# Performance work log

Measured on AMD Instinct MI355X. Metric: run time of the kernel, lower is better.

The kernel has to match this reference:

```python
import jax, jax.numpy as jnp
import numpy as np

N_NODES = 50000
N_EDGES = 1_600_000
DIMS = [512, 2048, 1024, 512]  # input, hiddens..., output
NEG_SLOPE = 0.2
EPS = 1e-12


def setup_inputs() -> dict:
    key = jax.random.key(0)
    ks = jax.random.split(key, 12)
    inp = {
        "x": jax.random.normal(ks[0], (N_NODES, DIMS[0]), dtype=jnp.float32),
        "edge_row": jax.random.randint(ks[1], (N_EDGES,), 0, N_NODES, dtype=jnp.int32),
        "edge_col": jax.random.randint(ks[2], (N_EDGES,), 0, N_NODES, dtype=jnp.int32),
        "edge_val": jax.random.uniform(ks[3], (N_EDGES,), dtype=jnp.float32),
    }
    # GraphConvolution params per layer: W [d_in, d_out], b [d_out]
    for i in range(len(DIMS) - 1):
        d_in, d_out = DIMS[i], DIMS[i + 1]
        scale = 1.0 / np.sqrt(d_in)
        inp[f"W{i}"] = jax.random.uniform(ks[4 + 2 * i], (d_in, d_out), minval=-scale, maxval=scale, dtype=jnp.float32)
        inp[f"b{i}"] = jnp.zeros((d_out,), dtype=jnp.float32)
    return inp


def _spmm(edge_row, edge_col, edge_val, h):
    # out[i] = sum_{e: row[e]==i} val[e] * h[col[e]]   (sparse adj @ h)
    msgs = edge_val[:, None] * h[edge_col]  # [E, d]
    return jax.ops.segment_sum(msgs, edge_row, num_segments=N_NODES)


def reference(x, edge_row, edge_col, edge_val, W0, b0, W1, b1, W2, b2):
    Ws = [W0, W1, W2]
    bs = [b0, b1, b2]
    # F.normalize: L2-normalize each row
    norm = jnp.sqrt(jnp.sum(x * x, axis=1, keepdims=True))
    h = x / jnp.maximum(norm, EPS)
    n_layers = len(Ws)
    for i in range(n_layers):
        support = h @ Ws[i]                                  # [N, d_out]
        h = _spmm(edge_row, edge_col, edge_val, support) + bs[i]
        if i != n_layers - 1:
            # dropout is identity at inference; leaky_relu(0.2)
            h = jnp.where(h >= 0, h, NEG_SLOPE * h)
    return h
```

## Files before the change

### kernel.cpp

```cpp
#include <hip/hip_runtime.h>
#include <stdint.h>

#define N_NODES 50000
#define N_EDGES 1600000
#define NCB 13

typedef __attribute__((ext_vector_type(8))) short bf16x8;
typedef __attribute__((ext_vector_type(4))) float f32x4;
typedef __attribute__((ext_vector_type(8))) unsigned short u16x8;

__device__ __forceinline__ float b2f(unsigned short u) {
  union { unsigned int i; float f; } v; v.i = ((unsigned int)u) << 16; return v.f;
}
__device__ __forceinline__ unsigned short f2b(float f) {
  union { float f; unsigned int i; } v; v.f = f;
  unsigned int u = v.i;
  u += 0x7fffu + ((u >> 16) & 1u);
  return (unsigned short)(u >> 16);
}

__device__ __forceinline__ void load_lds16(const void* g, void* l) {
  __builtin_amdgcn_global_load_lds(
      (const __attribute__((address_space(1))) unsigned int*)g,
      (__attribute__((address_space(3))) unsigned int*)l, 16, 0, 0);
}

__global__ __launch_bounds__(256) void normalize_k(const float* __restrict__ x,
                                                   unsigned short* __restrict__ out) {
  int lane = threadIdx.x & 63;
  int row = blockIdx.x * 4 + (threadIdx.x >> 6);
  const float* p = x + (size_t)row * 512 + lane * 8;
  float4 a = ((const float4*)p)[0];
  float4 b = ((const float4*)p)[1];
  float ss = a.x*a.x + a.y*a.y + a.z*a.z + a.w*a.w
           + b.x*b.x + b.y*b.y + b.z*b.z + b.w*b.w;
#pragma unroll
  for (int off = 1; off < 64; off <<= 1) ss += __shfl_xor(ss, off, 64);
  float s = 1.0f / fmaxf(sqrtf(ss), 1e-12f);
  u16x8 o;
  o[0]=f2b(a.x*s); o[1]=f2b(a.y*s); o[2]=f2b(a.z*s); o[3]=f2b(a.w*s);
  o[4]=f2b(b.x*s); o[5]=f2b(b.y*s); o[6]=f2b(b.z*s); o[7]=f2b(b.w*s);
  *(u16x8*)(out + (size_t)row * 512 + lane * 8) = o;
}

__global__ __launch_bounds__(256) void hist2_k(const int* __restrict__ er, const int* __restrict__ ec,
                                               int* __restrict__ h2) {
  int i = blockIdx.x * 256 + threadIdx.x;
  if (i < N_EDGES) atomicAdd(&h2[er[i] * NCB + (ec[i] >> 12)], 1);
}

__global__ __launch_bounds__(256) void scan1_k(const int* __restrict__ deg, int* __restrict__ out,
                                               int* __restrict__ csum, int n) {
  __shared__ int sd[256];
  int t = threadIdx.x;
  int base = blockIdx.x * 1024;
  int v[4], s = 0;
#pragma unroll
  for (int j = 0; j < 4; ++j) {
    int idx = base + t * 4 + j;
    v[j] = (idx < n) ? deg[idx] : 0;
    s += v[j];
  }
  sd[t] = s;
  __syncthreads();
  for (int off = 1; off < 256; off <<= 1) {
    int xx = (t >= off) ? sd[t - off] : 0;
    __syncthreads();
    sd[t] += xx;
    __syncthreads();
  }
  if (t == 255) csum[blockIdx.x] = sd[255];
  int run = sd[t] - s;
#pragma unroll
  for (int j = 0; j < 4; ++j) {
    int idx = base + t * 4 + j;
    if (idx < n) out[idx] = run;
    run += v[j];
  }
}

__global__ __launch_bounds__(256) void scan2p_k(int* __restrict__ csum, int n) {
  __shared__ int sd[256];
  int t = threadIdx.x;
  int v[3], s = 0;
#pragma unroll
  for (int j = 0; j < 3; ++j) {
    int idx = t * 3 + j;
    v[j] = (idx < n) ? csum[idx] : 0;
    s += v[j];
  }
  sd[t] = s;
  __syncthreads();
  for (int off = 1; off < 256; off <<= 1) {
    int xx = (t >= off) ? sd[t - off] : 0;
    __syncthreads();
    sd[t] += xx;
    __syncthreads();
  }
  int run = sd[t] - s;
#pragma unroll
  for (int j = 0; j < 3; ++j) {
    int idx = t * 3 + j;
    if (idx < n) csum[idx] = run;
    run += v[j];
  }
}

__global__ __launch_bounds__(256) void scan3_k(int* __restrict__ out, const int* __restrict__ csum, int n) {
  int i = blockIdx.x * 256 + threadIdx.x;
  if (i < n) out[i] += csum[i >> 10];
}

__global__ __launch_bounds__(256) void extract_k(const int* __restrict__ rs2, int* __restrict__ rs_s) {
  int i = blockIdx.x * 256 + threadIdx.x;
  if (i < N_NODES) rs_s[i] = rs2[i * NCB];
  if (i == N_NODES) rs_s[i] = N_EDGES;
}

__global__ __launch_bounds__(256) void scatter2_k(const int* __restrict__ er, const int* __restrict__ ec,
    const float* __restrict__ ev, int* __restrict__ head2, int2* __restrict__ ep) {
  int i = blockIdx.x * 256 + threadIdx.x;
  if (i < N_EDGES) {
    int r = er[i], c = ec[i];
    int p = atomicAdd(&head2[r * NCB + (c >> 12)], 1);
    ep[p] = make_int2(c, __float_as_int(ev[i]));
  }
}

__global__ __launch_bounds__(256) void wconv3_k(const float* __restrict__ W0f,
                                                const float* __restrict__ W1f,
                                                const float* __restrict__ W2f,
                                                unsigned short* __restrict__ w0t,
                                                unsigned short* __restrict__ w1t,
                                                unsigned short* __restrict__ w2t) {
  const int S0 = 512 * 2048;
  const int S1 = 2048 * 1024;
  const int S2 = 1024 * 512;
  int i = blockIdx.x * 256 + threadIdx.x;
  if (i < S0) {
    int n = i / 512, k = i - n * 512;
    w0t[i] = f2b(W0f[(size_t)k * 2048 + n]);
  } else if (i < S0 + S1) {
    int j = i - S0;
    int n = j / 2048, k = j - n * 2048;
    w1t[j] = f2b(W1f[(size_t)k * 1024 + n]);
  } else if (i < S0 + S1 + S2) {
    int j = i - S0 - S1;
    int n = j / 1024, k = j - n * 1024;
    w2t[j] = f2b(W2f[(size_t)k * 512 + n]);
  }
}

template <int D, int MODE>
__global__ __launch_bounds__(256) void spmm_k(const unsigned short* __restrict__ in,
    const int* __restrict__ rs, const int2* __restrict__ ep,
    const float* __restrict__ bias, void* __restrict__ outv) {
  constexpr int NS = D / 512;
  int lane = threadIdx.x & 63;
  int blk = blockIdx.x;
  int slice = (NS == 1) ? 0 : (blk / 12500);
  int rowg = (NS == 1) ? blk : (blk - slice * 12500);
  int row = rowg * 4 + (threadIdx.x >> 6);
  int e0 = rs[row];
  int e1 = rs[row + 1];
  float acc[8] = {0.f, 0.f, 0.f, 0.f, 0.f, 0.f, 0.f, 0.f};
  const unsigned short* base = in + (size_t)slice * 512 + (size_t)lane * 8;
  int e = e0;
  for (; e + 4 <= e1; e += 4) {
    int2 p0 = ep[e];
    int2 p1 = ep[e + 1];
    int2 p2 = ep[e + 2];
    int2 p3 = ep[e + 3];
    unsigned c0 = (unsigned)p0.x < N_NODES ? (unsigned)p0.x : 0u;
    unsigned c1 = (unsigned)p1.x < N_NODES ? (unsigned)p1.x : 0u;
    unsigned c2 = (unsigned)p2.x < N_NODES ? (unsigned)p2.x : 0u;
    unsigned c3 = (unsigned)p3.x < N_NODES ? (unsigned)p3.x : 0u;
    u16x8 u0 = *(const u16x8*)(base + (size_t)c0 * D);
    u16x8 u1 = *(const u16x8*)(base + (size_t)c1 * D);
    u16x8 u2 = *(const u16x8*)(base + (size_t)c2 * D);
    u16x8 u3 = *(const u16x8*)(base + (size_t)c3 * D);
    float v0 = __int_as_float(p0.y), v1 = __int_as_float(p1.y);
    float v2 = __int_as_float(p2.y), v3 = __int_as_float(p3.y);
#pragma unroll
    for (int h = 0; h < 8; ++h) acc[h] = fmaf(v0, b2f(u0[h]), acc[h]);
#pragma unroll
    for (int h = 0; h < 8; ++h) acc[h] = fmaf(v1, b2f(u1[h]), acc[h]);
#pragma unroll
    for (int h = 0; h < 8; ++h) acc[h] = fmaf(v2, b2f(u2[h]), acc[h]);
#pragma unroll
    for (int h = 0; h < 8; ++h) acc[h] = fmaf(v3, b2f(u3[h]), acc[h]);
  }
  for (; e < e1; ++e) {
    int2 p = ep[e];
    unsigned c = (unsigned)p.x < N_NODES ? (unsigned)p.x : 0u;
    u16x8 u = *(const u16x8*)(base + (size_t)c * D);
    float v = __int_as_float(p.y);
#pragma unroll
    for (int h = 0; h < 8; ++h) acc[h] = fmaf(v, b2f(u[h]), acc[h]);
  }
  size_t obase = (size_t)row * D + (size_t)slice * 512 + lane * 8;
  int bbase = slice * 512 + lane * 8;
  if (MODE == 2) {
    float* out = (float*)outv;
#pragma unroll
    for (int j = 0; j < 8; ++j) out[obase + j] = acc[j] + bias[bbase + j];
  } else {
    unsigned short* out = (unsigned short*)outv;
    u16x8 o;
#pragma unroll
    for (int h = 0; h < 8; ++h) {
      float xo = acc[h];
      if (MODE == 1) {
        xo += bias[bbase + h];
        xo = xo >= 0.f ? xo : 0.2f * xo;
      }
      o[h] = f2b(xo);
    }
    *(u16x8*)(out + obase) = o;
  }
}

template <bool BIAS_RELU>
__global__ __launch_bounds__(256) void gemm_bt_k(
    const unsigned short* __restrict__ A, const unsigned short* __restrict__ BT,
    const float* __restrict__ bias, unsigned short* __restrict__ C,
    int M, int N, int K, int gx) {
  __shared__ __align__(16) unsigned short sA[128 * 32];
  __shared__ __align__(16) unsigned short sB[128 * 32];
  int nwg = gridDim.x;
  int id = blockIdx.x;
  int q = nwg >> 3, r = nwg & 7;
  int xcd = id & 7, pos = id >> 3;
  int nid = (xcd < r ? xcd * (q + 1) : r * (q + 1) + (xcd - r) * q) + pos;
  const int G = 8;
  int gsz = gx * G;
  int grp = nid / gsz;
  int rem = nid - grp * gsz;
  int bx = rem % gx;
  int by = grp * G + rem / gx;

  int tid = threadIdx.x;
  int lane = tid & 63;
  int wid = tid >> 6;
  int wm = (wid & 1) * 64;
  int wn = (wid >> 1) * 64;
  int mblk = by * 128;
  int nblk = bx * 128;
  const unsigned short* Bb = BT + (size_t)nblk * K;
  int c0 = tid, c1 = tid + 256;
  int ar0 = c0 >> 2, ac0 = (c0 & 3) * 8;
  int ar1 = c1 >> 2, ac1 = (c1 & 3) * 8;
  int ra0 = mblk + ar0; if (ra0 > M - 1) ra0 = M - 1;
  int ra1 = mblk + ar1; if (ra1 > M - 1) ra1 = M - 1;
  f32x4 acc[4][4] = {};
  for (int k0 = 0; k0 < K; k0 += 32) {
    load_lds16(A + (size_t)ra0 * K + k0 + ac0, &sA[c0 * 8]);
    load_lds16(A + (size_t)ra1 * K + k0 + ac1, &sA[c1 * 8]);
    load_lds16(Bb + (size_t)ar0 * K + k0 + ac0, &sB[c0 * 8]);
    load_lds16(Bb + (size_t)ar1 * K + k0 + ac1, &sB[c1 * 8]);
    __syncthreads();
    bf16x8 af[4], bfr[4];
    int kq = (lane >> 4) * 8;
    int mr = wm + (lane & 15);
    int nr = wn + (lane & 15);
#pragma unroll
    for (int i = 0; i < 4; ++i) af[i] = *(const bf16x8*)&sA[(mr + i * 16) * 32 + kq];
#pragma unroll
    for (int j = 0; j < 4; ++j) bfr[j] = *(const bf16x8*)&sB[(nr + j * 16) * 32 + kq];
#pragma unroll
    for (int i = 0; i < 4; ++i)
#pragma unroll
      for (int j = 0; j < 4; ++j)
        acc[i][j] = __builtin_amdgcn_mfma_f32_16x16x32_bf16(af[i], bfr[j], acc[i][j], 0, 0, 0);
    __syncthreads();
  }
  int quad = lane >> 4;
  int lc = lane & 15;
#pragma unroll
  for (int i = 0; i < 4; ++i) {
#pragma unroll
    for (int r2 = 0; r2 < 4; ++r2) {
      int gm = mblk + wm + i * 16 + quad * 4 + r2;
      if (gm < M) {
#pragma unroll
        for (int j = 0; j < 4; ++j) {
          int gn = nblk + wn + j * 16 + lc;
          float v = acc[i][j][r2];
          if (BIAS_RELU) { v += bias[gn]; v = v >= 0.f ? v : 0.2f * v; }
          C[(size_t)gm * N + gn] = f2b(v);
        }
      }
    }
  }
}

extern "C" void kernel_launch(void* const* d_in, const int* in_sizes, int n_in,
                              void* d_out, int out_size, void* d_ws, size_t ws_size,
                              hipStream_t stream) {
  (void)in_sizes; (void)n_in; (void)out_size;
  const float* x  = (const float*)d_in[0];
  const int* erow = (const int*)d_in[1];
  const int* ecol = (const int*)d_in[2];
  const float* ev = (const float*)d_in[3];
  const float* W0 = (const float*)d_in[4];
  const float* b0 = (const float*)d_in[5];
  const float* W1 = (const float*)d_in[6];
  const float* b1 = (const float*)d_in[7];
  const float* W2 = (const float*)d_in[8];
  const float* b2 = (const float*)d_in[9];

  const size_t POOL_T1 = 256000000;
  const size_t POOL_T2 = 204800000;
  const size_t POOL_T3 = 153600000;
  const size_t META = 12800000 + 200064 + 7340032;
  int tier = (ws_size >= POOL_T1 + META) ? 1 : (ws_size >= POOL_T2 + META) ? 2 : 3;
  size_t pool_sz = (tier == 1) ? POOL_T1 : (tier == 2) ? POOL_T2 : POOL_T3;

  char* ws = (char*)d_ws;
  int2*  ep   = (int2*)(ws + pool_sz);
  int*   rs_s = (int*)(ws + pool_sz + 12800000);
  unsigned short* w0t = (unsigned short*)(ws + pool_sz + 12800000 + 200064);
  unsigned short* w1t = w0t + (size_t)2048 * 512;
  unsigned short* w2t = w1t + (size_t)1024 * 2048;
  int* rs2   = (int*)(ws);
  int* csum  = (int*)(ws + 2600064);
  int* head2 = (int*)(ws + 2604160);
  unsigned short* u = (unsigned short*)d_out;

  hipMemsetAsync(rs2, 0, 2600064, stream);
  hist2_k<<<6250, 256, 0, stream>>>(erow, ecol, rs2);
  scan1_k<<<635, 256, 0, stream>>>(rs2, rs2, csum, N_NODES * NCB);
  scan2p_k<<<1, 256, 0, stream>>>(csum, 635);
  scan3_k<<<2540, 256, 0, stream>>>(rs2, csum, N_NODES * NCB);
  extract_k<<<196, 256, 0, stream>>>(rs2, rs_s);
  hipMemcpyAsync(head2, rs2, (size_t)N_NODES * NCB * 4, hipMemcpyDeviceToDevice, stream);
  scatter2_k<<<6250, 256, 0, stream>>>(erow, ecol, ev, head2, ep);

  wconv3_k<<<14336, 256, 0, stream>>>(W0, W1, W2, w0t, w1t, w2t);

  if (tier == 1) {
    unsigned short* h1        = (unsigned short*)(ws);
    unsigned short* norm_out  = (unsigned short*)(ws);
    unsigned short* spmm0_out = (unsigned short*)(ws + 204800000);
    unsigned short* h2        = (unsigned short*)(ws);
    unsigned short* vbuf      = (unsigned short*)(ws + 102400000);
    normalize_k<<<12500, 256, 0, stream>>>(x, norm_out);
    spmm_k<512, 0><<<12500, 256, 0, stream>>>(norm_out, rs_s, ep, nullptr, spmm0_out);
    gemm_bt_k<true ><<<16 * 391, 256, 0, stream>>>(spmm0_out, w0t, b0, h1, N_NODES, 2048, 512, 16);
    gemm_bt_k<false><<<8 * 391, 256, 0, stream>>>(h1, w1t, nullptr, u, N_NODES, 1024, 2048, 8);
    spmm_k<1024, 1><<<25000, 256, 0, stream>>>(u, rs_s, ep, b1, h2);
    gemm_bt_k<false><<<4 * 391, 256, 0, stream>>>(h2, w2t, nullptr, vbuf, N_NODES, 512, 1024, 4);
    spmm_k<512, 2><<<12500, 256, 0, stream>>>(vbuf, rs_s, ep, b2, (float*)d_out);
  } else {
    int nchunk = (tier == 2) ? 2 : 4;
    int crows = (tier == 2) ? 25000 : 12500;
    int ytiles = (tier == 2) ? 196 : 98;
    unsigned short* norm_out  = (unsigned short*)(ws);
    unsigned short* spmm0_out = (unsigned short*)(ws + 51200000);
    unsigned short* h1chunk   = (unsigned short*)(ws + 102400000);
    unsigned short* h2        = (unsigned short*)(ws);
    unsigned short* vbuf      = (unsigned short*)(ws + 102400000);
    normalize_k<<<12500, 256, 0, stream>>>(x, norm_out);
    spmm_k<512, 0><<<12500, 256, 0, stream>>>(norm_out, rs_s, ep, nullptr, spmm0_out);
    for (int c = 0; c < nchunk; ++c) {
      const unsigned short* a0 = spmm0_out + (size_t)c * crows * 512;
      unsigned short* uc = u + (size_t)c * crows * 1024;
      gemm_bt_k<true ><<<16 * ytiles, 256, 0, stream>>>(a0, w0t, b0, h1chunk, crows, 2048, 512, 16);
      gemm_bt_k<false><<<8 * ytiles, 256, 0, stream>>>(h1chunk, w1t, nullptr, uc, crows, 1024, 2048, 8);
    }
    spmm_k<1024, 1><<<25000, 256, 0, stream>>>(u, rs_s, ep, b1, h2);
    gemm_bt_k<false><<<4 * 391, 256, 0, stream>>>(h2, w2t, nullptr, vbuf, N_NODES, 512, 1024, 4);
    spmm_k<512, 2><<<12500, 256, 0, stream>>>(vbuf, rs_s, ep, b2, (float*)d_out);
  }
}
```

Before: 1.813 ms.

## Restructure SpMM into column-block-ordered traversal with feature chunks per block

```diff
diff --git a/kernel.cpp b/kernel.cpp
--- a/kernel.cpp
+++ b/kernel.cpp
@@ -111,10 +111,14 @@
   if (i < n) out[i] += csum[i >> 10];
 }
 
-__global__ __launch_bounds__(256) void extract_k(const int* __restrict__ rs2, int* __restrict__ rs_s) {
+__global__ __launch_bounds__(256) void extract_k(const int* __restrict__ rs2c, int* __restrict__ rs_s,
+                                                 int* __restrict__ rs2w) {
   int i = blockIdx.x * 256 + threadIdx.x;
-  if (i < N_NODES) rs_s[i] = rs2[i * NCB];
-  if (i == N_NODES) rs_s[i] = N_EDGES;
+  if (i < N_NODES) rs_s[i] = rs2c[i * NCB];
+  if (i == N_NODES) {
+    rs_s[i] = N_EDGES;
+    rs2w[(size_t)N_NODES * NCB] = N_EDGES;
+  }
 }
 
 __global__ __launch_bounds__(256) void scatter2_k(const int* __restrict__ er, const int* __restrict__ ec,
@@ -152,71 +156,92 @@
 }
 
 template <int D, int MODE>
-__global__ __launch_bounds__(256) void spmm_k(const unsigned short* __restrict__ in,
-    const int* __restrict__ rs, const int2* __restrict__ ep,
+__global__ __launch_bounds__(256) void spmm_c_k(const unsigned short* __restrict__ in,
+    const int* __restrict__ rs2, const int2* __restrict__ ep,
     const float* __restrict__ bias, void* __restrict__ outv) {
-  constexpr int NS = D / 512;
+  constexpr int CF = D / 8;
+  constexpr int FPL = CF / 64;
   int lane = threadIdx.x & 63;
-  int blk = blockIdx.x;
-  int slice = (NS == 1) ? 0 : (blk / 12500);
-  int rowg = (NS == 1) ? blk : (blk - slice * 12500);
-  int row = rowg * 4 + (threadIdx.x >> 6);
-  int e0 = rs[row];
-  int e1 = rs[row + 1];
-  float acc[8] = {0.f, 0.f, 0.f, 0.f, 0.f, 0.f, 0.f, 0.f};
-  const unsigned short* base = in + (size_t)slice * 512 + (size_t)lane * 8;
-  int e = e0;
-  for (; e + 4 <= e1; e += 4) {
-    int2 p0 = ep[e];
-    int2 p1 = ep[e + 1];
-    int2 p2 = ep[e + 2];
-    int2 p3 = ep[e + 3];
-    unsigned c0 = (unsigned)p0.x < N_NODES ? (unsigned)p0.x : 0u;
-    unsigned c1 = (unsigned)p1.x < N_NODES ? (unsigned)p1.x : 0u;
-    unsigned c2 = (unsigned)p2.x < N_NODES ? (unsigned)p2.x : 0u;
-    unsigned c3 = (unsigned)p3.x < N_NODES ? (unsigned)p3.x : 0u;
-    u16x8 u0 = *(const u16x8*)(base + (size_t)c0 * D);
-    u16x8 u1 = *(const u16x8*)(base + (size_t)c1 * D);
-    u16x8 u2 = *(const u16x8*)(base + (size_t)c2 * D);
-    u16x8 u3 = *(const u16x8*)(base + (size_t)c3 * D);
-    float v0 = __int_as_float(p0.y), v1 = __int_as_float(p1.y);
-    float v2 = __int_as_float(p2.y), v3 = __int_as_float(p3.y);
-#pragma unroll
-    for (int h = 0; h < 8; ++h) acc[h] = fmaf(v0, b2f(u0[h]), acc[h]);
-#pragma unroll
-    for (int h = 0; h < 8; ++h) acc[h] = fmaf(v1, b2f(u1[h]), acc[h]);
-#pragma unroll
-    for (int h = 0; h < 8; ++h) acc[h] = fmaf(v2, b2f(u2[h]), acc[h]);
-#pragma unroll
-    for (int h = 0; h < 8; ++h) acc[h] = fmaf(v3, b2f(u3[h]), acc[h]);
-  }
-  for (; e < e1; ++e) {
-    int2 p = ep[e];
-    unsigned c = (unsigned)p.x < N_NODES ? (unsigned)p.x : 0u;
-    u16x8 u = *(const u16x8*)(base + (size_t)c * D);
-    float v = __int_as_float(p.y);
-#pragma unroll
-    for (int h = 0; h < 8; ++h) acc[h] = fmaf(v, b2f(u[h]), acc[h]);
-  }
-  size_t obase = (size_t)row * D + (size_t)slice * 512 + lane * 8;
-  int bbase = slice * 512 + lane * 8;
-  if (MODE == 2) {
-    float* out = (float*)outv;
-#pragma unroll
-    for (int j = 0; j < 8; ++j) out[obase + j] = acc[j] + bias[bbase + j];
-  } else {
-    unsigned short* out = (unsigned short*)outv;
-    u16x8 o;
-#pragma unroll
-    for (int h = 0; h < 8; ++h) {
-      float xo = acc[h];
-      if (MODE == 1) {
-        xo += bias[bbase + h];
-        xo = xo >= 0.f ? xo : 0.2f * xo;
+  int wid = threadIdx.x >> 6;
+  int chunk = blockIdx.x & 7;
+  int rowg = blockIdx.x >> 3;
+  int rbase = (rowg * 4 + wid) * 8;
+  float acc[8][FPL];
+#pragma unroll
+  for (int j = 0; j < 8; ++j)
+#pragma unroll
+    for (int f = 0; f < FPL; ++f) acc[j][f] = 0.f;
+  const char* hb = (const char*)in + (chunk * CF + lane * FPL) * 2;
+  const unsigned int rowBytes = D * 2;
+
+  for (int cb = 0; cb < NCB; ++cb) {
+#pragma unroll 1
+    for (int j = 0; j < 8; ++j) {
+      int row = rbase + j;
+      if (row >= N_NODES) continue;
+      int e0 = rs2[row * NCB + cb];
+      int e1 = rs2[row * NCB + cb + 1];
+      int e = e0;
+      for (; e + 2 <= e1; e += 2) {
+        int2 pa = ep[e];
+        int2 pb = ep[e + 1];
+        unsigned ca = (unsigned)pa.x < N_NODES ? (unsigned)pa.x : 0u;
+        unsigned cb2 = (unsigned)pb.x < N_NODES ? (unsigned)pb.x : 0u;
+        float va = __int_as_float(pa.y);
+        float vb = __int_as_float(pb.y);
+        if (FPL == 2) {
+          unsigned int wa = *(const unsigned int*)(hb + (size_t)(ca * rowBytes));
+          unsigned int wb = *(const unsigned int*)(hb + (size_t)(cb2 * rowBytes));
+          union { unsigned int i; float f; } l0, h0, l1, h1;
+          l0.i = wa << 16; h0.i = wa & 0xffff0000u;
+          l1.i = wb << 16; h1.i = wb & 0xffff0000u;
+          acc[j][0] = fmaf(va, l0.f, acc[j][0]);
+          acc[j][1] = fmaf(va, h0.f, acc[j][1]);
+          acc[j][0] = fmaf(vb, l1.f, acc[j][0]);
+          acc[j][1] = fmaf(vb, h1.f, acc[j][1]);
+        } else {
+          float f0 = b2f(*(const unsigned short*)(hb + (size_t)(ca * rowBytes)));
+          float f1 = b2f(*(const unsigned short*)(hb + (size_t)(cb2 * rowBytes)));
+          acc[j][0] = fmaf(va, f0, acc[j][0]);
+          acc[j][0] = fmaf(vb, f1, acc[j][0]);
+        }
       }
-      o[h] = f2b(xo);
+      if (e < e1) {
+        int2 p = ep[e];
+        unsigned c = (unsigned)p.x < N_NODES ? (unsigned)p.x : 0u;
+        float v = __int_as_float(p.y);
+        if (FPL == 2) {
+          unsigned int w = *(const unsigned int*)(hb + (size_t)(c * rowBytes));
+          union { unsigned int i; float f; } lo, hi;
+          lo.i = w << 16; hi.i = w & 0xffff0000u;
+          acc[j][0] = fmaf(v, lo.f, acc[j][0]);
+          acc[j][1] = fmaf(v, hi.f, acc[j][1]);
+        } else {
+          float f0 = b2f(*(const unsigned short*)(hb + (size_t)(c * rowBytes)));
+          acc[j][0] = fmaf(v, f0, acc[j][0]);
+        }
+      }
     }
-    *(u16x8*)(out + obase) = o;
+  }
+
+#pragma unroll 1
+  for (int j = 0; j < 8; ++j) {
+    int row = rbase + j;
+    if (row >= N_NODES) continue;
+    if (MODE == 2) {
+      float* out = (float*)outv;
+      out[(size_t)row * D + chunk * CF + lane] = acc[j][0] + bias[chunk * CF + lane];
+    } else if (MODE == 1) {
+      int fb = chunk * CF + lane * 2;
+      float x0 = acc[j][0] + bias[fb];
+      float x1 = acc[j][1] + bias[fb + 1];
+      x0 = x0 >= 0.f ? x0 : 0.2f * x0;
+      x1 = x1 >= 0.f ? x1 : 0.2f * x1;
+      unsigned int o = (unsigned int)f2b(x0) | ((unsigned int)f2b(x1) << 16);
+      *(unsigned int*)((unsigned short*)outv + (size_t)row * D + fb) = o;
+    } else {
+      ((unsigned short*)outv)[(size_t)row * D + chunk * CF + lane] = f2b(acc[j][0]);
+    }
   }
 }
 
@@ -312,7 +337,8 @@
   const size_t POOL_T1 = 256000000;
   const size_t POOL_T2 = 204800000;
   const size_t POOL_T3 = 153600000;
-  const size_t META = 12800000 + 200064 + 7340032;
+  const size_t RS2_SZ = 2600128;
+  const size_t META = 12800000 + 200064 + 7340032 + RS2_SZ;
   int tier = (ws_size >= POOL_T1 + META) ? 1 : (ws_size >= POOL_T2 + META) ? 2 : 3;
   size_t pool_sz = (tier == 1) ? POOL_T1 : (tier == 2) ? POOL_T2 : POOL_T3;
 
@@ -322,9 +348,9 @@
   unsigned short* w0t = (unsigned short*)(ws + pool_sz + 12800000 + 200064);
   unsigned short* w1t = w0t + (size_t)2048 * 512;
   unsigned short* w2t = w1t + (size_t)1024 * 2048;
-  int* rs2   = (int*)(ws);
+  int*   rs2  = (int*)(ws + pool_sz + 12800000 + 200064 + 7340032);
+  int* head2 = (int*)(ws);
   int* csum  = (int*)(ws + 2600064);
-  int* head2 = (int*)(ws + 2604160);
   unsigned short* u = (unsigned short*)d_out;
 
   hipMemsetAsync(rs2, 0, 2600064, stream);
@@ -332,11 +358,13 @@
   scan1_k<<<635, 256, 0, stream>>>(rs2, rs2, csum, N_NODES * NCB);
   scan2p_k<<<1, 256, 0, stream>>>(csum, 635);
   scan3_k<<<2540, 256, 0, stream>>>(rs2, csum, N_NODES * NCB);
-  extract_k<<<196, 256, 0, stream>>>(rs2, rs_s);
+  extract_k<<<196, 256, 0, stream>>>(rs2, rs_s, rs2);
   hipMemcpyAsync(head2, rs2, (size_t)N_NODES * NCB * 4, hipMemcpyDeviceToDevice, stream);
   scatter2_k<<<6250, 256, 0, stream>>>(erow, ecol, ev, head2, ep);
 
   wconv3_k<<<14336, 256, 0, stream>>>(W0, W1, W2, w0t, w1t, w2t);
+
+  const int SPMM_GRID = 8 * 1563;
 
   if (tier == 1) {
     unsigned short* h1        = (unsigned short*)(ws);
@@ -345,12 +373,12 @@
     unsigned short* h2        = (unsigned short*)(ws);
     unsigned short* vbuf      = (unsigned short*)(ws + 102400000);
     normalize_k<<<12500, 256, 0, stream>>>(x, norm_out);
-    spmm_k<512, 0><<<12500, 256, 0, stream>>>(norm_out, rs_s, ep, nullptr, spmm0_out);
+    spmm_c_k<512, 0><<<SPMM_GRID, 256, 0, stream>>>(norm_out, rs2, ep, nullptr, spmm0_out);
     gemm_bt_k<true ><<<16 * 391, 256, 0, stream>>>(spmm0_out, w0t, b0, h1, N_NODES, 2048, 512, 16);
     gemm_bt_k<false><<<8 * 391, 256, 0, stream>>>(h1, w1t, nullptr, u, N_NODES, 1024, 2048, 8);
-    spmm_k<1024, 1><<<25000, 256, 0, stream>>>(u, rs_s, ep, b1, h2);
+    spmm_c_k<1024, 1><<<SPMM_GRID, 256, 0, stream>>>(u, rs2, ep, b1, h2);
     gemm_bt_k<false><<<4 * 391, 256, 0, stream>>>(h2, w2t, nullptr, vbuf, N_NODES, 512, 1024, 4);
-    spmm_k<512, 2><<<12500, 256, 0, stream>>>(vbuf, rs_s, ep, b2, (float*)d_out);
+    spmm_c_k<512, 2><<<SPMM_GRID, 256, 0, stream>>>(vbuf, rs2, ep, b2, (float*)d_out);
   } else {
     int nchunk = (tier == 2) ? 2 : 4;
     int crows = (tier == 2) ? 25000 : 12500;
@@ -361,15 +389,15 @@
     unsigned short* h2        = (unsigned short*)(ws);
     unsigned short* vbuf      = (unsigned short*)(ws + 102400000);
     normalize_k<<<12500, 256, 0, stream>>>(x, norm_out);
-    spmm_k<512, 0><<<12500, 256, 0, stream>>>(norm_out, rs_s, ep, nullptr, spmm0_out);
+    spmm_c_k<512, 0><<<SPMM_GRID, 256, 0, stream>>>(norm_out, rs2, ep, nullptr, spmm0_out);
     for (int c = 0; c < nchunk; ++c) {
       const unsigned short* a0 = spmm0_out + (size_t)c * crows * 512;
       unsigned short* uc = u + (size_t)c * crows * 1024;
       gemm_bt_k<true ><<<16 * ytiles, 256, 0, stream>>>(a0, w0t, b0, h1chunk, crows, 2048, 512, 16);
       gemm_bt_k<false><<<8 * ytiles, 256, 0, stream>>>(h1chunk, w1t, nullptr, uc, crows, 1024, 2048, 8);
     }
-    spmm_k<1024, 1><<<25000, 256, 0, stream>>>(u, rs_s, ep, b1, h2);
+    spmm_c_k<1024, 1><<<SPMM_GRID, 256, 0, stream>>>(u, rs2, ep, b1, h2);
     gemm_bt_k<false><<<4 * 391, 256, 0, stream>>>(h2, w2t, nullptr, vbuf, N_NODES, 512, 1024, 4);
-    spmm_k<512, 2><<<12500, 256, 0, stream>>>(vbuf, rs_s, ep, b2, (float*)d_out);
-  }
-}
+    spmm_c_k<512, 2><<<SPMM_GRID, 256, 0, stream>>>(vbuf, rs2, ep, b2, (float*)d_out);
+  }
+}
```

After: 3.743 ms. 106% more time.
